# Kernel optimization log

Measured on AMD Instinct MI355X. Metric: run time of the kernel, lower is better.

## Reference

```python
import jax, jax.numpy as jnp
import numpy as np

D_MODEL = 512
NUM_HEADS = 8
DEPTH = D_MODEL // NUM_HEADS


def setup_inputs() -> dict:
    key = jax.random.key(0)
    kx, kq, kk, kv, ko = jax.random.split(key, 5)
    scale = 1.0 / np.sqrt(D_MODEL)
    return {
        "x": jax.random.normal(kx, (4, 2048, D_MODEL), dtype=jnp.float32),
        "W_q": jax.random.normal(kq, (D_MODEL, D_MODEL), dtype=jnp.float32) * scale,
        "W_k": jax.random.normal(kk, (D_MODEL, D_MODEL), dtype=jnp.float32) * scale,
        "W_v": jax.random.normal(kv, (D_MODEL, D_MODEL), dtype=jnp.float32) * scale,
        "W_o": jax.random.normal(ko, (D_MODEL, D_MODEL), dtype=jnp.float32) * scale,
    }


def reference(x, W_q, W_k, W_v, W_o):
    B, S, _ = x.shape
    # nn.Linear with weight W: y = x @ W.T
    def split_heads(t):
        return t.reshape(B, S, NUM_HEADS, DEPTH).transpose(0, 2, 1, 3)  # [B,H,S,D]
    Q = split_heads(x @ W_q.T)
    K = split_heads(x @ W_k.T)
    V = split_heads(x @ W_v.T)
    b = -jnp.log(jnp.asarray(S, dtype=jnp.float32))  # -log(seq_len) bias
    inv_sqrt_dk = 1.0 / jnp.sqrt(jnp.asarray(DEPTH, dtype=jnp.float32))
    qk = jnp.einsum('bhqd,bhkd->bhqk', Q, K) * inv_sqrt_dk
    attn = jax.nn.sigmoid(qk + b)  # non-softmax sigmoid attention
    out = jnp.einsum('bhqk,bhkd->bhqd', attn, V)
    out = out.transpose(0, 2, 1, 3).reshape(B, S, D_MODEL)
    return out @ W_o.T
```

## Files before the change

kernel.cpp:

```cpp
#include <hip/hip_runtime.h>
#include <stdint.h>

typedef _Float16 f16x8 __attribute__((ext_vector_type(8)));
typedef _Float16 f16x4 __attribute__((ext_vector_type(4)));
typedef __fp16 h16x2 __attribute__((ext_vector_type(2)));
typedef float f32x4 __attribute__((ext_vector_type(4)));

#define SEQ 2048
#define NHEADS 8

#define GLOAD_LDS16(gp, lp)                                                        \
  __builtin_amdgcn_global_load_lds(                                                \
      (const __attribute__((address_space(1))) void*)(uintptr_t)(const void*)(gp), \
      (__attribute__((address_space(3))) void*)(uintptr_t)(void*)(lp), 16, 0, 0)

__device__ __forceinline__ f16x4 pack4(float a, float b, float c, float d) {
  h16x2 lo = __builtin_amdgcn_cvt_pkrtz(a, b);
  h16x2 hi = __builtin_amdgcn_cvt_pkrtz(c, d);
  f16x4 o;
  o.x = (_Float16)lo.x; o.y = (_Float16)lo.y;
  o.z = (_Float16)hi.x; o.w = (_Float16)hi.y;
  return o;
}

__global__ void cvt_all_kernel(const float* __restrict__ x, const float* __restrict__ wq,
                               const float* __restrict__ wk, const float* __restrict__ wv,
                               const float* __restrict__ wo, _Float16* __restrict__ xh,
                               _Float16* __restrict__ wh) {
  int i = blockIdx.x * 256 + threadIdx.x;
  const float* src;
  _Float16* dst;
  int off;
  if (i < 1048576) {
    src = x; dst = xh; off = i;
  } else {
    int j = i - 1048576;
    int sel = j >> 16;
    off = j & 65535;
    src = (sel == 0) ? wq : (sel == 1) ? wk : (sel == 2) ? wv : wo;
    dst = wh + (size_t)sel * 262144;
  }
  float4 v = ((const float4*)src)[off];
  ((f16x4*)dst)[off] = pack4(v.x, v.y, v.z, v.w);
}

__device__ __forceinline__ void gemm_tile_bt(const _Float16* __restrict__ A,
                                             const _Float16* __restrict__ B,
                                             int m0, int n0,
                                             _Float16* As, _Float16* Bs,
                                             f32x4 (&acc)[4][4]) {
  const int tid = threadIdx.x;
  const int w = tid >> 6, lane = tid & 63;
  const int wr = w >> 1, wc = w & 1;
  const int lrow = lane & 15, q = lane >> 4;
  const int snb = w * 32 + (lane >> 3);
  const int scb = lane & 7;

#pragma unroll
  for (int i = 0; i < 4; ++i)
#pragma unroll
    for (int j = 0; j < 4; ++j)
#pragma unroll
      for (int r = 0; r < 4; ++r) acc[i][j][r] = 0.f;

  for (int kt = 0; kt < 8; ++kt) {
    __syncthreads();
#pragma unroll
    for (int t = 0; t < 4; ++t) {
      int n = snb + t * 8;
      int cbg = scb ^ (n & 7);
      GLOAD_LDS16(A + (size_t)(m0 + n) * 512 + kt * 64 + cbg * 8,
                  As + (w * 32 + t * 8) * 64);
      GLOAD_LDS16(B + (size_t)(n0 + n) * 512 + kt * 64 + cbg * 8,
                  Bs + (w * 32 + t * 8) * 64);
    }
    __syncthreads();

    f16x8 af[4][2], bfr[4][2];
#pragma unroll
    for (int i = 0; i < 4; ++i) {
      int m = wr * 64 + i * 16 + lrow;
#pragma unroll
      for (int kk = 0; kk < 2; ++kk) {
        int cb = (kk * 4 + q) ^ (m & 7);
        af[i][kk] = *(const f16x8*)(As + m * 64 + cb * 8);
      }
    }
#pragma unroll
    for (int j = 0; j < 4; ++j) {
      int n = wc * 64 + j * 16 + lrow;
#pragma unroll
      for (int kk = 0; kk < 2; ++kk) {
        int cb = (kk * 4 + q) ^ (n & 7);
        bfr[j][kk] = *(const f16x8*)(Bs + n * 64 + cb * 8);
      }
    }
#pragma unroll
    for (int i = 0; i < 4; ++i)
#pragma unroll
      for (int j = 0; j < 4; ++j) {
        acc[i][j] = __builtin_amdgcn_mfma_f32_16x16x32_f16(af[i][0], bfr[j][0], acc[i][j], 0, 0, 0);
        acc[i][j] = __builtin_amdgcn_mfma_f32_16x16x32_f16(af[i][1], bfr[j][1], acc[i][j], 0, 0, 0);
      }
  }
}

__global__ __launch_bounds__(256, 2) void qkv_kernel(
    const _Float16* __restrict__ xb, const _Float16* __restrict__ Wq,
    const _Float16* __restrict__ Wk, const _Float16* __restrict__ Wv,
    _Float16* __restrict__ Qo, _Float16* __restrict__ Ko, _Float16* __restrict__ Vto) {
  __shared__ _Float16 pool[17408];
  _Float16* As = pool;
  _Float16* Bs = pool + 8192;
  const int z = blockIdx.z;
  f32x4 acc[4][4];
  const int tid = threadIdx.x, w = tid >> 6, lane = tid & 63;
  const int wr = w >> 1, wc = w & 1, lcol = lane & 15, q = lane >> 4;

  if (z < 2) {
    const int m0 = blockIdx.y * 128;
    const int n0 = blockIdx.x * 128;
    gemm_tile_bt((z == 0) ? Wq : Wk, xb, m0, n0, As, Bs, acc);
    _Float16* outp = (z == 0) ? Qo : Ko;
    __syncthreads();
#pragma unroll
    for (int i = 0; i < 4; ++i) {
      int cl = wr * 64 + i * 16 + q * 4;
#pragma unroll
      for (int j = 0; j < 4; ++j) {
        int s = wc * 64 + j * 16 + lcol;
        *(f16x4*)(pool + s * 136 + cl) =
            pack4(acc[i][j][0], acc[i][j][1], acc[i][j][2], acc[i][j][3]);
      }
    }
    __syncthreads();
#pragma unroll
    for (int it = 0; it < 16; ++it) {
      int srow = it * 8 + (tid >> 5);
      int ch = tid & 31;
      f16x4 v = *(const f16x4*)(pool + srow * 136 + ch * 4);
      *(f16x4*)(outp + (size_t)(n0 + srow) * 512 + m0 + ch * 4) = v;
    }
  } else {
    const int m0 = blockIdx.x * 128;
    const int n0 = blockIdx.y * 128;
    gemm_tile_bt(xb, Wv, m0, n0, As, Bs, acc);
    const int bb = m0 >> 11, sl0 = m0 & 2047;
    __syncthreads();
#pragma unroll
    for (int i = 0; i < 4; ++i) {
      int s0 = wr * 64 + i * 16 + q * 4;
#pragma unroll
      for (int j = 0; j < 4; ++j) {
        int c = wc * 64 + j * 16 + lcol;
        *(f16x4*)(pool + c * 136 + s0) =
            pack4(acc[i][j][0], acc[i][j][1], acc[i][j][2], acc[i][j][3]);
      }
    }
    __syncthreads();
#pragma unroll
    for (int it = 0; it < 16; ++it) {
      int crow = it * 8 + (tid >> 5);
      int ch = tid & 31;
      int cg = n0 + crow, h = cg >> 6, d = cg & 63;
      f16x4 v = *(const f16x4*)(pool + crow * 136 + ch * 4);
      *(f16x4*)(Vto + ((size_t)((bb * NHEADS + h) * 64 + d)) * SEQ + sl0 + ch * 4) = v;
    }
  }
}

__global__ __launch_bounds__(256, 2) void attn_kernel(
    const _Float16* __restrict__ Qw, const _Float16* __restrict__ Kw,
    const _Float16* __restrict__ Vtw, _Float16* __restrict__ Ow) {
  __shared__ _Float16 lds[32768];
  _Float16* Ks = lds;
  _Float16* Vts = lds + 8192;
  _Float16* Ps = lds + 16384;
  _Float16* Qs = Ps;

  const int tid = threadIdx.x, w = tid >> 6, lane = tid & 63;
  const int wr = w >> 1, wc = w & 1, lrow = lane & 15, q = lane >> 4;

  const int L = blockIdx.x;
  const int xcd = L & 7, slot = L >> 3;
  const int bh = xcd * 4 + (slot >> 4), qt = slot & 15;
  const int b = bh >> 3, h = bh & 7;
  const int q0 = qt * 128;

  const _Float16* Qp = Qw + ((size_t)(b * SEQ + q0)) * 512 + h * 64;
  const _Float16* Kp = Kw + ((size_t)b * SEQ) * 512 + h * 64;
  const _Float16* Vp = Vtw + (size_t)bh * 64 * SEQ;

  const int snb = w * 32 + (lane >> 3), scb = lane & 7;
  const int vnb = w * 16 + (lane >> 4), vcb = lane & 15;

#pragma unroll
  for (int t = 0; t < 4; ++t) {
    int n = snb + t * 8;
    int cbg = scb ^ (n & 7);
    GLOAD_LDS16(Qp + (size_t)n * 512 + cbg * 8, Qs + (w * 32 + t * 8) * 64);
  }
  __syncthreads();

  f16x8 qa[4][2];
#pragma unroll
  for (int i = 0; i < 4; ++i) {
    int m = wr * 64 + i * 16 + lrow;
#pragma unroll
    for (int kk = 0; kk < 2; ++kk) {
      int cb = (kk * 4 + q) ^ (m & 7);
      qa[i][kk] = *(const f16x8*)(Qs + m * 64 + cb * 8);
    }
  }

  f32x4 oacc[4][2];
#pragma unroll
  for (int i = 0; i < 4; ++i)
#pragma unroll
    for (int j = 0; j < 2; ++j)
#pragma unroll
      for (int r = 0; r < 4; ++r) oacc[i][j][r] = 0.f;

  const float c1 = 0.18033688011112042f;

  for (int kt = 0; kt < 16; ++kt) {
    __syncthreads();
#pragma unroll
    for (int t = 0; t < 4; ++t) {
      int n = snb + t * 8;
      int cbg = scb ^ (n & 7);
      GLOAD_LDS16(Kp + (size_t)(kt * 128 + n) * 512 + cbg * 8, Ks + (w * 32 + t * 8) * 64);
    }
#pragma unroll
    for (int t = 0; t < 4; ++t) {
      int nv = vnb + t * 4;
      int cbg = vcb ^ (nv & 15);
      GLOAD_LDS16(Vp + (size_t)nv * SEQ + kt * 128 + cbg * 8, Vts + (w * 16 + t * 4) * 128);
    }
    __syncthreads();

    f32x4 sacc[4][4];
#pragma unroll
    for (int i = 0; i < 4; ++i)
#pragma unroll
      for (int j = 0; j < 4; ++j)
#pragma unroll
        for (int r = 0; r < 4; ++r) sacc[i][j][r] = 0.f;
    f16x8 kb[4][2];
#pragma unroll
    for (int j = 0; j < 4; ++j) {
      int n = wc * 64 + j * 16 + lrow;
#pragma unroll
      for (int kk = 0; kk < 2; ++kk) {
        int cb = (kk * 4 + q) ^ (n & 7);
        kb[j][kk] = *(const f16x8*)(Ks + n * 64 + cb * 8);
      }
    }
#pragma unroll
    for (int i = 0; i < 4; ++i)
#pragma unroll
      for (int j = 0; j < 4; ++j) {
        sacc[i][j] = __builtin_amdgcn_mfma_f32_16x16x32_f16(qa[i][0], kb[j][0], sacc[i][j], 0, 0, 0);
        sacc[i][j] = __builtin_amdgcn_mfma_f32_16x16x32_f16(qa[i][1], kb[j][1], sacc[i][j], 0, 0, 0);
      }

#pragma unroll
    for (int i = 0; i < 4; ++i) {
      int prow0 = wr * 64 + i * 16 + q * 4;
#pragma unroll
      for (int j = 0; j < 4; ++j) {
        int pcol = wc * 64 + j * 16 + lrow;
        int cb = pcol >> 3, ci = pcol & 7;
#pragma unroll
        for (int r = 0; r < 4; ++r) {
          int prow = prow0 + r;
          float wp = __builtin_amdgcn_exp2f(__builtin_fmaf(sacc[i][j][r], c1, -1.0f));
          float u = wp * -0.0009765625f;
          float zz = __builtin_fmaf(u, __builtin_fmaf(u, 1.0f + u, 1.0f), 1.0f);
          Ps[prow * 128 + ((cb ^ (prow & 15)) << 3) + ci] = (_Float16)(wp * zz);
        }
      }
    }
    __syncthreads();

#pragma unroll
    for (int ks = 0; ks < 4; ++ks) {
      f16x8 pa[4], vb[2];
#pragma unroll
      for (int i2 = 0; i2 < 4; ++i2) {
        int m = wr * 64 + i2 * 16 + lrow;
        int cb = (ks * 4 + q) ^ (m & 15);
        pa[i2] = *(const f16x8*)(Ps + m * 128 + cb * 8);
      }
#pragma unroll
      for (int j2 = 0; j2 < 2; ++j2) {
        int n = wc * 32 + j2 * 16 + lrow;
        int cb = (ks * 4 + q) ^ (n & 15);
        vb[j2] = *(const f16x8*)(Vts + n * 128 + cb * 8);
      }
#pragma unroll
      for (int i2 = 0; i2 < 4; ++i2)
#pragma unroll
        for (int j2 = 0; j2 < 2; ++j2)
          oacc[i2][j2] = __builtin_amdgcn_mfma_f32_16x16x32_f16(pa[i2], vb[j2], oacc[i2][j2], 0, 0, 0);
    }
  }

  __syncthreads();
  _Float16* Ob = Ps;
#pragma unroll
  for (int i2 = 0; i2 < 4; ++i2) {
#pragma unroll
    for (int j2 = 0; j2 < 2; ++j2) {
      int d = wc * 32 + j2 * 16 + lrow;
#pragma unroll
      for (int r = 0; r < 4; ++r) {
        int row = wr * 64 + i2 * 16 + q * 4 + r;
        Ob[row * 72 + d] = (_Float16)(oacc[i2][j2][r] * 0.0009765625f);
      }
    }
  }
  __syncthreads();
#pragma unroll
  for (int it = 0; it < 8; ++it) {
    int row = it * 16 + (tid >> 4);
    int ch = tid & 15;
    f16x4 v = *(const f16x4*)(Ob + row * 72 + ch * 4);
    *(f16x4*)(Ow + (size_t)(b * SEQ + q0 + row) * 512 + h * 64 + ch * 4) = v;
  }
}

__global__ __launch_bounds__(256, 2) void oproj_kernel(
    const _Float16* __restrict__ A, const _Float16* __restrict__ Wo,
    float* __restrict__ out) {
  __shared__ _Float16 As[128 * 64];
  __shared__ _Float16 Bs[128 * 64];
  const int m0 = blockIdx.x * 128, n0 = blockIdx.y * 128;
  f32x4 acc[4][4];
  gemm_tile_bt(A, Wo, m0, n0, As, Bs, acc);

  const int tid = threadIdx.x, w = tid >> 6, lane = tid & 63;
  const int wr = w >> 1, wc = w & 1, lcol = lane & 15, q = lane >> 4;
#pragma unroll
  for (int i = 0; i < 4; ++i) {
    int gm0 = m0 + wr * 64 + i * 16 + q * 4;
#pragma unroll
    for (int j = 0; j < 4; ++j) {
      int gn = n0 + wc * 64 + j * 16 + lcol;
#pragma unroll
      for (int r = 0; r < 4; ++r)
        out[(size_t)(gm0 + r) * 512 + gn] = acc[i][j][r];
    }
  }
}

extern "C" void kernel_launch(void* const* d_in, const int* in_sizes, int n_in,
                              void* d_out, int out_size, void* d_ws, size_t ws_size,
                              hipStream_t stream) {
  const float* x = (const float*)d_in[0];
  const float* Wq = (const float*)d_in[1];
  const float* Wk = (const float*)d_in[2];
  const float* Wv = (const float*)d_in[3];
  const float* Wo = (const float*)d_in[4];
  float* out = (float*)d_out;
  char* ws = (char*)d_ws;

  _Float16* xh = (_Float16*)(ws + 0);
  _Float16* wh = (_Float16*)(ws + 8388608);
  _Float16* Qw = (_Float16*)(ws + 10485760);
  _Float16* Kw = (_Float16*)(ws + 18874368);
  _Float16* Vtw = (_Float16*)(ws + 27262976);
  _Float16* Ow = (_Float16*)(ws + 35651584);

  _Float16* wqh = wh;
  _Float16* wkh = wh + 262144;
  _Float16* wvh = wh + 524288;
  _Float16* woh = wh + 786432;

  cvt_all_kernel<<<5120, 256, 0, stream>>>(x, Wq, Wk, Wv, Wo, xh, wh);
  qkv_kernel<<<dim3(64, 4, 3), 256, 0, stream>>>(xh, wqh, wkh, wvh, Qw, Kw, Vtw);
  attn_kernel<<<512, 256, 0, stream>>>(Qw, Kw, Vtw, Ow);
  oproj_kernel<<<dim3(64, 4), 256, 0, stream>>>(Ow, woh, out);
}
```

Baseline: 169.7 us.

## Split QKV into fused Q/K kernel sharing x tile, separate V kernel, transpose S MFMA

The Q and K projections now run in one kernel that loads each x tile once and multiplies it against both W_q and W_k, holding two accumulator sets. The V projection moves to its own kernel launch. In attention, the score MFMA operands are swapped so each lane holds four consecutive keys, which lets the sigmoid results be packed and stored as one f16x4 write instead of four scalar writes. The sigmoid correction polynomial is also simplified. In exchange, the Q/K kernel needs more registers and LDS, and there is one extra kernel launch.

```diff
diff --git a/kernel.cpp b/kernel.cpp
--- a/kernel.cpp
+++ b/kernel.cpp
@@ -105,67 +105,130 @@
   }
 }
 
-__global__ __launch_bounds__(256, 2) void qkv_kernel(
+__global__ __launch_bounds__(256, 2) void qk_kernel(
     const _Float16* __restrict__ xb, const _Float16* __restrict__ Wq,
-    const _Float16* __restrict__ Wk, const _Float16* __restrict__ Wv,
-    _Float16* __restrict__ Qo, _Float16* __restrict__ Ko, _Float16* __restrict__ Vto) {
-  __shared__ _Float16 pool[17408];
-  _Float16* As = pool;
-  _Float16* Bs = pool + 8192;
-  const int z = blockIdx.z;
-  f32x4 acc[4][4];
+    const _Float16* __restrict__ Wk, _Float16* __restrict__ Qo,
+    _Float16* __restrict__ Ko) {
+  __shared__ _Float16 pool[24576];
+  _Float16* xs = pool;
+  _Float16* wqs = pool + 8192;
+  _Float16* wks = pool + 16384;
+  const int n0 = blockIdx.x * 128;
+  const int m0 = blockIdx.y * 128;
   const int tid = threadIdx.x, w = tid >> 6, lane = tid & 63;
-  const int wr = w >> 1, wc = w & 1, lcol = lane & 15, q = lane >> 4;
-
-  if (z < 2) {
-    const int m0 = blockIdx.y * 128;
-    const int n0 = blockIdx.x * 128;
-    gemm_tile_bt((z == 0) ? Wq : Wk, xb, m0, n0, As, Bs, acc);
+  const int wr = w >> 1, wc = w & 1, lrow = lane & 15, q = lane >> 4;
+  const int snb = w * 32 + (lane >> 3), scb = lane & 7;
+
+  f32x4 accq[4][4], acck[4][4];
+#pragma unroll
+  for (int i = 0; i < 4; ++i)
+#pragma unroll
+    for (int j = 0; j < 4; ++j)
+#pragma unroll
+      for (int r = 0; r < 4; ++r) { accq[i][j][r] = 0.f; acck[i][j][r] = 0.f; }
+
+  for (int kt = 0; kt < 8; ++kt) {
+    __syncthreads();
+#pragma unroll
+    for (int t = 0; t < 4; ++t) {
+      int n = snb + t * 8;
+      int cbg = scb ^ (n & 7);
+      GLOAD_LDS16(xb + (size_t)(m0 + n) * 512 + kt * 64 + cbg * 8, xs + (w * 32 + t * 8) * 64);
+      GLOAD_LDS16(Wq + (size_t)(n0 + n) * 512 + kt * 64 + cbg * 8, wqs + (w * 32 + t * 8) * 64);
+      GLOAD_LDS16(Wk + (size_t)(n0 + n) * 512 + kt * 64 + cbg * 8, wks + (w * 32 + t * 8) * 64);
+    }
+    __syncthreads();
+
+    f16x8 af[4][2], bq[4][2], bk[4][2];
+#pragma unroll
+    for (int i = 0; i < 4; ++i) {
+      int m = wr * 64 + i * 16 + lrow;
+#pragma unroll
+      for (int kk = 0; kk < 2; ++kk) {
+        int cb = (kk * 4 + q) ^ (m & 7);
+        af[i][kk] = *(const f16x8*)(xs + m * 64 + cb * 8);
+      }
+    }
+#pragma unroll
+    for (int j = 0; j < 4; ++j) {
+      int n = wc * 64 + j * 16 + lrow;
+#pragma unroll
+      for (int kk = 0; kk < 2; ++kk) {
+        int cb = (kk * 4 + q) ^ (n & 7);
+        bq[j][kk] = *(const f16x8*)(wqs + n * 64 + cb * 8);
+        bk[j][kk] = *(const f16x8*)(wks + n * 64 + cb * 8);
+      }
+    }
+#pragma unroll
+    for (int i = 0; i < 4; ++i)
+#pragma unroll
+      for (int j = 0; j < 4; ++j) {
+        accq[i][j] = __builtin_amdgcn_mfma_f32_16x16x32_f16(af[i][0], bq[j][0], accq[i][j], 0, 0, 0);
+        accq[i][j] = __builtin_amdgcn_mfma_f32_16x16x32_f16(af[i][1], bq[j][1], accq[i][j], 0, 0, 0);
+        acck[i][j] = __builtin_amdgcn_mfma_f32_16x16x32_f16(af[i][0], bk[j][0], acck[i][j], 0, 0, 0);
+        acck[i][j] = __builtin_amdgcn_mfma_f32_16x16x32_f16(af[i][1], bk[j][1], acck[i][j], 0, 0, 0);
+      }
+  }
+
+#pragma unroll
+  for (int z = 0; z < 2; ++z) {
+    __syncthreads();
+#pragma unroll
+    for (int i = 0; i < 4; ++i) {
+      int s0 = wr * 64 + i * 16 + q * 4;
+#pragma unroll
+      for (int j = 0; j < 4; ++j) {
+        int c = wc * 64 + j * 16 + lrow;
+#pragma unroll
+        for (int r = 0; r < 4; ++r)
+          pool[(s0 + r) * 136 + c] =
+              (_Float16)((z == 0) ? accq[i][j][r] : acck[i][j][r]);
+      }
+    }
+    __syncthreads();
     _Float16* outp = (z == 0) ? Qo : Ko;
-    __syncthreads();
-#pragma unroll
-    for (int i = 0; i < 4; ++i) {
-      int cl = wr * 64 + i * 16 + q * 4;
-#pragma unroll
-      for (int j = 0; j < 4; ++j) {
-        int s = wc * 64 + j * 16 + lcol;
-        *(f16x4*)(pool + s * 136 + cl) =
-            pack4(acc[i][j][0], acc[i][j][1], acc[i][j][2], acc[i][j][3]);
-      }
-    }
-    __syncthreads();
 #pragma unroll
     for (int it = 0; it < 16; ++it) {
       int srow = it * 8 + (tid >> 5);
       int ch = tid & 31;
       f16x4 v = *(const f16x4*)(pool + srow * 136 + ch * 4);
-      *(f16x4*)(outp + (size_t)(n0 + srow) * 512 + m0 + ch * 4) = v;
-    }
-  } else {
-    const int m0 = blockIdx.x * 128;
-    const int n0 = blockIdx.y * 128;
-    gemm_tile_bt(xb, Wv, m0, n0, As, Bs, acc);
-    const int bb = m0 >> 11, sl0 = m0 & 2047;
-    __syncthreads();
-#pragma unroll
-    for (int i = 0; i < 4; ++i) {
-      int s0 = wr * 64 + i * 16 + q * 4;
-#pragma unroll
-      for (int j = 0; j < 4; ++j) {
-        int c = wc * 64 + j * 16 + lcol;
-        *(f16x4*)(pool + c * 136 + s0) =
-            pack4(acc[i][j][0], acc[i][j][1], acc[i][j][2], acc[i][j][3]);
-      }
-    }
-    __syncthreads();
-#pragma unroll
-    for (int it = 0; it < 16; ++it) {
-      int crow = it * 8 + (tid >> 5);
-      int ch = tid & 31;
-      int cg = n0 + crow, h = cg >> 6, d = cg & 63;
-      f16x4 v = *(const f16x4*)(pool + crow * 136 + ch * 4);
-      *(f16x4*)(Vto + ((size_t)((bb * NHEADS + h) * 64 + d)) * SEQ + sl0 + ch * 4) = v;
-    }
+      *(f16x4*)(outp + (size_t)(m0 + srow) * 512 + n0 + ch * 4) = v;
+    }
+  }
+}
+
+__global__ __launch_bounds__(256, 2) void v_kernel(
+    const _Float16* __restrict__ xb, const _Float16* __restrict__ Wv,
+    _Float16* __restrict__ Vto) {
+  __shared__ _Float16 pool[17408];
+  _Float16* As = pool;
+  _Float16* Bs = pool + 8192;
+  const int m0 = blockIdx.x * 128;
+  const int n0 = blockIdx.y * 128;
+  f32x4 acc[4][4];
+  gemm_tile_bt(xb, Wv, m0, n0, As, Bs, acc);
+  const int tid = threadIdx.x, w = tid >> 6, lane = tid & 63;
+  const int wr = w >> 1, wc = w & 1, lcol = lane & 15, q = lane >> 4;
+  const int bb = m0 >> 11, sl0 = m0 & 2047;
+  __syncthreads();
+#pragma unroll
+  for (int i = 0; i < 4; ++i) {
+    int s0 = wr * 64 + i * 16 + q * 4;
+#pragma unroll
+    for (int j = 0; j < 4; ++j) {
+      int c = wc * 64 + j * 16 + lcol;
+      *(f16x4*)(pool + c * 136 + s0) =
+          pack4(acc[i][j][0], acc[i][j][1], acc[i][j][2], acc[i][j][3]);
+    }
+  }
+  __syncthreads();
+#pragma unroll
+  for (int it = 0; it < 16; ++it) {
+    int crow = it * 8 + (tid >> 5);
+    int ch = tid & 31;
+    int cg = n0 + crow, h = cg >> 6, d = cg & 63;
+    f16x4 v = *(const f16x4*)(pool + crow * 136 + ch * 4);
+    *(f16x4*)(Vto + ((size_t)((bb * NHEADS + h) * 64 + d)) * SEQ + sl0 + ch * 4) = v;
   }
 }
 
@@ -239,13 +302,13 @@
     }
     __syncthreads();
 
-    f32x4 sacc[4][4];
-#pragma unroll
-    for (int i = 0; i < 4; ++i)
-#pragma unroll
-      for (int j = 0; j < 4; ++j)
-#pragma unroll
-        for (int r = 0; r < 4; ++r) sacc[i][j][r] = 0.f;
+    f32x4 st[4][4];
+#pragma unroll
+    for (int j = 0; j < 4; ++j)
+#pragma unroll
+      for (int i = 0; i < 4; ++i)
+#pragma unroll
+        for (int r = 0; r < 4; ++r) st[j][i][r] = 0.f;
     f16x8 kb[4][2];
 #pragma unroll
     for (int j = 0; j < 4; ++j) {
@@ -257,28 +320,30 @@
       }
     }
 #pragma unroll
-    for (int i = 0; i < 4; ++i)
+    for (int j = 0; j < 4; ++j)
+#pragma unroll
+      for (int i = 0; i < 4; ++i) {
+        st[j][i] = __builtin_amdgcn_mfma_f32_16x16x32_f16(kb[j][0], qa[i][0], st[j][i], 0, 0, 0);
+        st[j][i] = __builtin_amdgcn_mfma_f32_16x16x32_f16(kb[j][1], qa[i][1], st[j][i], 0, 0, 0);
+      }
+
+#pragma unroll
+    for (int i = 0; i < 4; ++i) {
+      int qrow = wr * 64 + i * 16 + lrow;
 #pragma unroll
       for (int j = 0; j < 4; ++j) {
-        sacc[i][j] = __builtin_amdgcn_mfma_f32_16x16x32_f16(qa[i][0], kb[j][0], sacc[i][j], 0, 0, 0);
-        sacc[i][j] = __builtin_amdgcn_mfma_f32_16x16x32_f16(qa[i][1], kb[j][1], sacc[i][j], 0, 0, 0);
-      }
-
-#pragma unroll
-    for (int i = 0; i < 4; ++i) {
-      int prow0 = wr * 64 + i * 16 + q * 4;
-#pragma unroll
-      for (int j = 0; j < 4; ++j) {
-        int pcol = wc * 64 + j * 16 + lrow;
-        int cb = pcol >> 3, ci = pcol & 7;
+        int kbase = wc * 64 + j * 16 + q * 4;
+        float p[4];
 #pragma unroll
         for (int r = 0; r < 4; ++r) {
-          int prow = prow0 + r;
-          float wp = __builtin_amdgcn_exp2f(__builtin_fmaf(sacc[i][j][r], c1, -1.0f));
-          float u = wp * -0.0009765625f;
-          float zz = __builtin_fmaf(u, __builtin_fmaf(u, 1.0f + u, 1.0f), 1.0f);
-          Ps[prow * 128 + ((cb ^ (prow & 15)) << 3) + ci] = (_Float16)(wp * zz);
+          float wp = __builtin_amdgcn_exp2f(__builtin_fmaf(st[j][i][r], c1, -1.0f));
+          float e = wp * 0.0009765625f;
+          float s1 = __builtin_fmaf(e, e, -e);
+          p[r] = __builtin_fmaf(wp, s1, wp);
         }
+        int kb8 = kbase >> 3;
+        *(f16x4*)(Ps + qrow * 128 + ((kb8 ^ (qrow & 15)) << 3) + (kbase & 7)) =
+            pack4(p[0], p[1], p[2], p[3]);
       }
     }
     __syncthreads();
@@ -378,7 +443,8 @@
   _Float16* woh = wh + 786432;
 
   cvt_all_kernel<<<5120, 256, 0, stream>>>(x, Wq, Wk, Wv, Wo, xh, wh);
-  qkv_kernel<<<dim3(64, 4, 3), 256, 0, stream>>>(xh, wqh, wkh, wvh, Qw, Kw, Vtw);
+  qk_kernel<<<dim3(4, 64), 256, 0, stream>>>(xh, wqh, wkh, Qw, Kw);
+  v_kernel<<<dim3(64, 4), 256, 0, stream>>>(xh, wvh, Vtw);
   attn_kernel<<<512, 256, 0, stream>>>(Qw, Kw, Vtw, Ow);
   oproj_kernel<<<dim3(64, 4), 256, 0, stream>>>(Ow, woh, out);
 }
```

New measurement: 166.2 us. 1.02x faster.

## Load K and V fragments directly from global into registers in attention

Applied to the files above, without the earlier changes.

The attention kernel stops staging K and V tiles in LDS. Each wave loads its MFMA operand fragments straight from global memory into registers, and the next K tile is prefetched while the current scores are processed. The score MFMA is transposed so each lane writes four consecutive P values as one packed f16x4 store, and the barriers are replaced by an LDS-only waitcnt plus s_barrier. This halves LDS usage and removes two barriers per tile, but reads K and V redundantly across waves through the cache with strided, uncoalesced global loads.

```diff
diff --git a/kernel.cpp b/kernel.cpp
--- a/kernel.cpp
+++ b/kernel.cpp
@@ -13,6 +13,11 @@
   __builtin_amdgcn_global_load_lds(                                                \
       (const __attribute__((address_space(1))) void*)(uintptr_t)(const void*)(gp), \
       (__attribute__((address_space(3))) void*)(uintptr_t)(void*)(lp), 16, 0, 0)
+
+__device__ __forceinline__ void barrier_lds() {
+  __builtin_amdgcn_s_waitcnt(0xc07f);
+  __builtin_amdgcn_s_barrier();
+}
 
 __device__ __forceinline__ f16x4 pack4(float a, float b, float c, float d) {
   h16x2 lo = __builtin_amdgcn_cvt_pkrtz(a, b);
@@ -172,11 +177,9 @@
 __global__ __launch_bounds__(256, 2) void attn_kernel(
     const _Float16* __restrict__ Qw, const _Float16* __restrict__ Kw,
     const _Float16* __restrict__ Vtw, _Float16* __restrict__ Ow) {
-  __shared__ _Float16 lds[32768];
-  _Float16* Ks = lds;
-  _Float16* Vts = lds + 8192;
-  _Float16* Ps = lds + 16384;
-  _Float16* Qs = Ps;
+  __shared__ _Float16 lds[16384];
+  _Float16* Ps = lds;
+  _Float16* Qs = lds;
 
   const int tid = threadIdx.x, w = tid >> 6, lane = tid & 63;
   const int wr = w >> 1, wc = w & 1, lrow = lane & 15, q = lane >> 4;
@@ -188,12 +191,12 @@
   const int q0 = qt * 128;
 
   const _Float16* Qp = Qw + ((size_t)(b * SEQ + q0)) * 512 + h * 64;
-  const _Float16* Kp = Kw + ((size_t)b * SEQ) * 512 + h * 64;
-  const _Float16* Vp = Vtw + (size_t)bh * 64 * SEQ;
+  const _Float16* Kt = Kw + ((size_t)b * SEQ) * 512 + h * 64 +
+                       (size_t)(wc * 64 + lrow) * 512 + q * 8;
+  const _Float16* Vt = Vtw + (size_t)bh * 64 * SEQ +
+                       (size_t)(wc * 32 + lrow) * SEQ + q * 8;
 
   const int snb = w * 32 + (lane >> 3), scb = lane & 7;
-  const int vnb = w * 16 + (lane >> 4), vcb = lane & 15;
-
 #pragma unroll
   for (int t = 0; t < 4; ++t) {
     int n = snb + t * 8;
@@ -213,6 +216,15 @@
     }
   }
 
+  f16x8 kb[4][2];
+#pragma unroll
+  for (int j = 0; j < 4; ++j)
+#pragma unroll
+    for (int kk = 0; kk < 2; ++kk)
+      kb[j][kk] = *(const f16x8*)(Kt + (size_t)(j * 16) * 512 + kk * 32);
+
+  barrier_lds();
+
   f32x4 oacc[4][2];
 #pragma unroll
   for (int i = 0; i < 4; ++i)
@@ -224,68 +236,61 @@
   const float c1 = 0.18033688011112042f;
 
   for (int kt = 0; kt < 16; ++kt) {
-    __syncthreads();
-#pragma unroll
-    for (int t = 0; t < 4; ++t) {
-      int n = snb + t * 8;
-      int cbg = scb ^ (n & 7);
-      GLOAD_LDS16(Kp + (size_t)(kt * 128 + n) * 512 + cbg * 8, Ks + (w * 32 + t * 8) * 64);
-    }
-#pragma unroll
-    for (int t = 0; t < 4; ++t) {
-      int nv = vnb + t * 4;
-      int cbg = vcb ^ (nv & 15);
-      GLOAD_LDS16(Vp + (size_t)nv * SEQ + kt * 128 + cbg * 8, Vts + (w * 16 + t * 4) * 128);
-    }
-    __syncthreads();
-
-    f32x4 sacc[4][4];
-#pragma unroll
-    for (int i = 0; i < 4; ++i)
+    f16x8 vb[2][4];
+#pragma unroll
+    for (int j2 = 0; j2 < 2; ++j2)
+#pragma unroll
+      for (int ks = 0; ks < 4; ++ks)
+        vb[j2][ks] = *(const f16x8*)(Vt + (size_t)(j2 * 16) * SEQ + kt * 128 + ks * 32);
+
+    f32x4 st[4][4];
+#pragma unroll
+    for (int j = 0; j < 4; ++j)
+#pragma unroll
+      for (int i = 0; i < 4; ++i)
+#pragma unroll
+        for (int r = 0; r < 4; ++r) st[j][i][r] = 0.f;
+#pragma unroll
+    for (int j = 0; j < 4; ++j)
+#pragma unroll
+      for (int i = 0; i < 4; ++i) {
+        st[j][i] = __builtin_amdgcn_mfma_f32_16x16x32_f16(kb[j][0], qa[i][0], st[j][i], 0, 0, 0);
+        st[j][i] = __builtin_amdgcn_mfma_f32_16x16x32_f16(kb[j][1], qa[i][1], st[j][i], 0, 0, 0);
+      }
+
+    {
+      int ktn = (kt + 1) & 15;
 #pragma unroll
       for (int j = 0; j < 4; ++j)
 #pragma unroll
-        for (int r = 0; r < 4; ++r) sacc[i][j][r] = 0.f;
-    f16x8 kb[4][2];
-#pragma unroll
-    for (int j = 0; j < 4; ++j) {
-      int n = wc * 64 + j * 16 + lrow;
-#pragma unroll
-      for (int kk = 0; kk < 2; ++kk) {
-        int cb = (kk * 4 + q) ^ (n & 7);
-        kb[j][kk] = *(const f16x8*)(Ks + n * 64 + cb * 8);
-      }
-    }
-#pragma unroll
-    for (int i = 0; i < 4; ++i)
+        for (int kk = 0; kk < 2; ++kk)
+          kb[j][kk] = *(const f16x8*)(Kt + (size_t)(ktn * 128 + j * 16) * 512 + kk * 32);
+    }
+
+#pragma unroll
+    for (int i = 0; i < 4; ++i) {
+      int qrow = wr * 64 + i * 16 + lrow;
 #pragma unroll
       for (int j = 0; j < 4; ++j) {
-        sacc[i][j] = __builtin_amdgcn_mfma_f32_16x16x32_f16(qa[i][0], kb[j][0], sacc[i][j], 0, 0, 0);
-        sacc[i][j] = __builtin_amdgcn_mfma_f32_16x16x32_f16(qa[i][1], kb[j][1], sacc[i][j], 0, 0, 0);
-      }
-
-#pragma unroll
-    for (int i = 0; i < 4; ++i) {
-      int prow0 = wr * 64 + i * 16 + q * 4;
-#pragma unroll
-      for (int j = 0; j < 4; ++j) {
-        int pcol = wc * 64 + j * 16 + lrow;
-        int cb = pcol >> 3, ci = pcol & 7;
+        int kbase = wc * 64 + j * 16 + q * 4;
+        float p[4];
 #pragma unroll
         for (int r = 0; r < 4; ++r) {
-          int prow = prow0 + r;
-          float wp = __builtin_amdgcn_exp2f(__builtin_fmaf(sacc[i][j][r], c1, -1.0f));
-          float u = wp * -0.0009765625f;
-          float zz = __builtin_fmaf(u, __builtin_fmaf(u, 1.0f + u, 1.0f), 1.0f);
-          Ps[prow * 128 + ((cb ^ (prow & 15)) << 3) + ci] = (_Float16)(wp * zz);
+          float wp = __builtin_amdgcn_exp2f(__builtin_fmaf(st[j][i][r], c1, -1.0f));
+          float e = wp * 0.0009765625f;
+          float s1 = __builtin_fmaf(e, e, -e);
+          p[r] = __builtin_fmaf(wp, s1, wp);
         }
-      }
-    }
-    __syncthreads();
+        int kb8 = kbase >> 3;
+        *(f16x4*)(Ps + qrow * 128 + ((kb8 ^ (qrow & 15)) << 3) + (kbase & 7)) =
+            pack4(p[0], p[1], p[2], p[3]);
+      }
+    }
+    barrier_lds();
 
 #pragma unroll
     for (int ks = 0; ks < 4; ++ks) {
-      f16x8 pa[4], vb[2];
+      f16x8 pa[4];
 #pragma unroll
       for (int i2 = 0; i2 < 4; ++i2) {
         int m = wr * 64 + i2 * 16 + lrow;
@@ -293,20 +298,14 @@
         pa[i2] = *(const f16x8*)(Ps + m * 128 + cb * 8);
       }
 #pragma unroll
-      for (int j2 = 0; j2 < 2; ++j2) {
-        int n = wc * 32 + j2 * 16 + lrow;
-        int cb = (ks * 4 + q) ^ (n & 15);
-        vb[j2] = *(const f16x8*)(Vts + n * 128 + cb * 8);
-      }
-#pragma unroll
       for (int i2 = 0; i2 < 4; ++i2)
 #pragma unroll
         for (int j2 = 0; j2 < 2; ++j2)
-          oacc[i2][j2] = __builtin_amdgcn_mfma_f32_16x16x32_f16(pa[i2], vb[j2], oacc[i2][j2], 0, 0, 0);
-    }
-  }
-
-  __syncthreads();
+          oacc[i2][j2] = __builtin_amdgcn_mfma_f32_16x16x32_f16(pa[i2], vb[j2][ks], oacc[i2][j2], 0, 0, 0);
+    }
+    barrier_lds();
+  }
+
   _Float16* Ob = Ps;
 #pragma unroll
   for (int i2 = 0; i2 < 4; ++i2) {
@@ -320,7 +319,7 @@
       }
     }
   }
-  __syncthreads();
+  barrier_lds();
 #pragma unroll
   for (int it = 0; it < 8; ++it) {
     int row = it * 16 + (tid >> 4);
```

Measured after the change: 178.9 us. 5.5% more time.
